# Performance work log

Hardware: AMD Instinct MI355X
Metric: run time of the kernel (lower is better)

The kernel has to match this reference:

```python
import jax, jax.numpy as jnp
import numpy as np

D = 256

def setup_inputs() -> dict:
    key = jax.random.key(0)
    ks = jax.random.split(key, 7)
    B, N = 4, 4096
    s = 1.0 / np.sqrt(D)
    return {
        "x": jax.random.normal(ks[0], (B, D, N), dtype=jnp.float32),
        "Wq": jax.random.normal(ks[1], (D, D), dtype=jnp.float32) * s,
        "bq": jax.random.normal(ks[2], (D,), dtype=jnp.float32) * s,
        "Wk": jax.random.normal(ks[3], (D, D), dtype=jnp.float32) * s,
        "bk": jax.random.normal(ks[4], (D,), dtype=jnp.float32) * s,
        "Wv": jax.random.normal(ks[5], (D, D), dtype=jnp.float32) * s,
        "bv": jax.random.normal(ks[6], (D,), dtype=jnp.float32) * s,
    }


def reference(x, Wq, bq, Wk, bk, Wv, bv):
    # x: (B, D, N) -> xt: (B, N, D)
    xt = jnp.swapaxes(x, 1, 2)
    q = xt @ Wq + bq  # (B, N, D)
    k = xt @ Wk + bk
    v = xt @ Wv + bv
    # full N x N attention, NO 1/sqrt(d) scaling (matches original)
    attn = jnp.einsum("bnd,bmd->bnm", q, k)
    attn = jax.nn.softmax(attn, axis=-1)
    out = jnp.einsum("bnm,bmd->bnd", attn, v)  # (B, N, D)
    return jnp.swapaxes(out, 1, 2)  # (B, D, N)
```

## Files before the change

### kernel.cpp

```cpp
#include <hip/hip_runtime.h>
#include <math.h>

#define Dd 256
#define Nn 4096
#define Bb 4
#define BQ 128
#define BK 128
#define SPLIT 2

typedef _Float16 f16;
typedef _Float16 half8 __attribute__((ext_vector_type(8)));
typedef _Float16 half4 __attribute__((ext_vector_type(4)));
typedef float f32x4 __attribute__((ext_vector_type(4)));

#define LOG2E 1.4426950408889634f

template <int CTRL>
__device__ __forceinline__ float dppf(float x) {
    int r = __builtin_amdgcn_update_dpp(0, __builtin_bit_cast(int, x),
                                        CTRL, 0xF, 0xF, false);
    return __builtin_bit_cast(float, r);
}
__device__ __forceinline__ float red16_max(float x) {
    x = fmaxf(x, dppf<0x128>(x));
    x = fmaxf(x, dppf<0x124>(x));
    x = fmaxf(x, dppf<0x122>(x));
    x = fmaxf(x, dppf<0x121>(x));
    return x;
}
__device__ __forceinline__ float red16_sum(float x) {
    x += dppf<0x128>(x); x += dppf<0x124>(x);
    x += dppf<0x122>(x); x += dppf<0x121>(x);
    return x;
}

__global__ __launch_bounds__(256) void wtrans(
    const float* __restrict__ Wq, const float* __restrict__ Wk,
    const float* __restrict__ Wv, f16* __restrict__ Wt)
{
    __shared__ float ld[64][65];
    const int which = blockIdx.y;
    const float* W = which == 0 ? Wq : (which == 1 ? Wk : Wv);
    const int tr = (blockIdx.x >> 2) * 64;
    const int tc = (blockIdx.x & 3) * 64;
    const int t = threadIdx.x;
    #pragma unroll
    for (int i = 0; i < 16; ++i) {
        int u = t + i * 256, r = u >> 6, c = u & 63;
        ld[r][c] = W[(size_t)(tr + r) * Dd + tc + c];
    }
    __syncthreads();
    f16* Wo = Wt + (size_t)which * Dd * Dd;
    #pragma unroll
    for (int i = 0; i < 16; ++i) {
        int u = t + i * 256, cp = u >> 6, rp = u & 63;
        Wo[(size_t)(tc + cp) * Dd + tr + rp] = (f16)ld[rp][cp];
    }
}

__global__ __launch_bounds__(256, 2) void qkv_mfma(
    const float* __restrict__ x, const f16* __restrict__ Wt,
    const float* __restrict__ bq, const float* __restrict__ bk,
    const float* __restrict__ bv,
    f16* __restrict__ Qh, f16* __restrict__ Kh, f16* __restrict__ Vth)
{
    __shared__ f16 xT[64][264];
    __shared__ float bs[256];
    const int t = threadIdx.x;
    const int wave = t >> 6, lane = t & 63, quad = lane >> 4, l15 = lane & 15;
    const int n0 = blockIdx.x * 64;
    const int b = blockIdx.y, which = blockIdx.z;
    const float* bias = which == 0 ? bq : (which == 1 ? bk : bv);
    bs[t] = bias[t];

    const float* xb = x + (size_t)b * Dd * Nn;
    #pragma unroll
    for (int i = 0; i < 16; ++i) {
        int u = t + i * 256, d = u >> 4, nq = (u & 15) * 4;
        float4 v4 = *(const float4*)&xb[(size_t)d * Nn + n0 + nq];
        xT[nq + 0][d] = (f16)v4.x; xT[nq + 1][d] = (f16)v4.y;
        xT[nq + 2][d] = (f16)v4.z; xT[nq + 3][d] = (f16)v4.w;
    }
    __syncthreads();

    half8 a[8];
    #pragma unroll
    for (int c = 0; c < 8; ++c)
        a[c] = *(const half8*)&xT[16 * wave + l15][c * 32 + quad * 8];

    f32x4 acc[16];
    #pragma unroll
    for (int dt = 0; dt < 16; ++dt) acc[dt] = (f32x4){0.f, 0.f, 0.f, 0.f};

    const f16* Wb = Wt + (size_t)which * Dd * Dd + (size_t)l15 * Dd + quad * 8;
    #pragma unroll
    for (int c = 0; c < 8; ++c) {
        #pragma unroll
        for (int dt = 0; dt < 16; ++dt) {
            half8 bfr = *(const half8*)(Wb + (size_t)dt * 16 * Dd + c * 32);
            acc[dt] = __builtin_amdgcn_mfma_f32_16x16x32_f16(a[c], bfr, acc[dt], 0, 0, 0);
        }
    }

    const int nrow = n0 + 16 * wave + quad * 4;
    if (which < 2) {
        f16* O = (which == 0 ? Qh : Kh) + ((size_t)b * Nn + nrow) * Dd;
        #pragma unroll
        for (int dt = 0; dt < 16; ++dt) {
            int col = dt * 16 + l15;
            float bvv = bs[col];
            #pragma unroll
            for (int r = 0; r < 4; ++r)
                O[(size_t)r * Dd + col] = (f16)(acc[dt][r] + bvv);
        }
    } else {
        f16* O = Vth + (size_t)b * Dd * Nn;
        #pragma unroll
        for (int dt = 0; dt < 16; ++dt) {
            int col = dt * 16 + l15;
            float bvv = bs[col];
            half4 o;
            #pragma unroll
            for (int r = 0; r < 4; ++r) o[r] = (f16)(acc[dt][r] + bvv);
            *(half4*)&O[(size_t)col * Nn + nrow] = o;
        }
    }
}

__global__ __launch_bounds__(512, 2) void attn_mfma(
    const f16* __restrict__ Qh, const f16* __restrict__ Kh,
    const f16* __restrict__ Vth, f16* __restrict__ Opart,
    float* __restrict__ mpart, float* __restrict__ lpart)
{
    __shared__ f16 Ks[BK][264];
    __shared__ f16 Ps[8][16][136];
    __shared__ float alpha_s[8][16];
    __shared__ float l_sh[8][16];

    const int t    = threadIdx.x;
    const int wave = t >> 6, lane = t & 63;
    const int quad = lane >> 4, l15 = lane & 15;
    const int b    = blockIdx.y;
    const int s    = blockIdx.z;
    const int q0   = blockIdx.x * BQ;
    const int qw   = q0 + wave * 16;
    const int kv0  = s * (Nn / SPLIT);

    half8 qf[8];
    const f16* Qrow = Qh + ((size_t)b * Nn + qw + l15) * Dd + quad * 8;
    #pragma unroll
    for (int c = 0; c < 8; ++c) {
        qf[c] = *(const half8*)(Qrow + c * 32);
        qf[c] = qf[c] * (f16)LOG2E;
    }

    f32x4 acc[16];
    #pragma unroll
    for (int n = 0; n < 16; ++n) acc[n] = (f32x4){0.f, 0.f, 0.f, 0.f};
    f32x4 m4 = {-1e30f, -1e30f, -1e30f, -1e30f};
    f32x4 l4 = {0.f, 0.f, 0.f, 0.f};

    const f16* Kb   = Kh + (size_t)b * Nn * Dd;
    const f16* Vrow = Vth + (size_t)b * Dd * Nn
                    + (size_t)(wave * 32 + l15) * Nn + quad * 8;

    for (int k0 = kv0; k0 < kv0 + Nn / SPLIT; k0 += BK) {
        half8 vbf[2][4];
        #pragma unroll
        for (int dt = 0; dt < 2; ++dt) {
            #pragma unroll
            for (int cbb = 0; cbb < 4; ++cbb)
                vbf[dt][cbb] = *(const half8*)(Vrow + (size_t)dt * 16 * Nn + k0 + cbb * 32);
        }

        __syncthreads();

        #pragma unroll
        for (int i = 0; i < 8; ++i) {
            int u = t + i * 512;
            int r = u >> 5, c = u & 31;
            *(half8*)&Ks[r][c * 8] =
                *(const half8*)(Kb + (size_t)(k0 + r) * Dd + c * 8);
        }
        __syncthreads();

        f32x4 S[8];
        #pragma unroll
        for (int cb = 0; cb < 8; ++cb) S[cb] = (f32x4){0.f, 0.f, 0.f, 0.f};
        #pragma unroll
        for (int c = 0; c < 8; ++c) {
            #pragma unroll
            for (int cb = 0; cb < 8; ++cb) {
                half8 kb = *(const half8*)&Ks[cb * 16 + l15][c * 32 + quad * 8];
                S[cb] = __builtin_amdgcn_mfma_f32_16x16x32_f16(qf[c], kb, S[cb], 0, 0, 0);
            }
        }

        f32x4 tmax = S[0];
        #pragma unroll
        for (int cb = 1; cb < 8; ++cb) {
            tmax.x = fmaxf(tmax.x, S[cb].x); tmax.y = fmaxf(tmax.y, S[cb].y);
            tmax.z = fmaxf(tmax.z, S[cb].z); tmax.w = fmaxf(tmax.w, S[cb].w);
        }
        tmax.x = red16_max(tmax.x); tmax.y = red16_max(tmax.y);
        tmax.z = red16_max(tmax.z); tmax.w = red16_max(tmax.w);
        f32x4 newm;
        newm.x = fmaxf(m4.x, tmax.x); newm.y = fmaxf(m4.y, tmax.y);
        newm.z = fmaxf(m4.z, tmax.z); newm.w = fmaxf(m4.w, tmax.w);
        f32x4 al;
        al.x = __builtin_amdgcn_exp2f(m4.x - newm.x);
        al.y = __builtin_amdgcn_exp2f(m4.y - newm.y);
        al.z = __builtin_amdgcn_exp2f(m4.z - newm.z);
        al.w = __builtin_amdgcn_exp2f(m4.w - newm.w);
        f32x4 P[8];
        #pragma unroll
        for (int cb = 0; cb < 8; ++cb) {
            P[cb].x = __builtin_amdgcn_exp2f(S[cb].x - newm.x);
            P[cb].y = __builtin_amdgcn_exp2f(S[cb].y - newm.y);
            P[cb].z = __builtin_amdgcn_exp2f(S[cb].z - newm.z);
            P[cb].w = __builtin_amdgcn_exp2f(S[cb].w - newm.w);
        }
        f32x4 rsum = P[0];
        #pragma unroll
        for (int cb = 1; cb < 8; ++cb) rsum += P[cb];
        rsum.x = red16_sum(rsum.x); rsum.y = red16_sum(rsum.y);
        rsum.z = red16_sum(rsum.z); rsum.w = red16_sum(rsum.w);
        l4 = l4 * al + rsum;
        m4 = newm;

        const int pr = quad * 4;
        #pragma unroll
        for (int cb = 0; cb < 8; ++cb) {
            Ps[wave][pr + 0][cb * 16 + l15] = (f16)P[cb].x;
            Ps[wave][pr + 1][cb * 16 + l15] = (f16)P[cb].y;
            Ps[wave][pr + 2][cb * 16 + l15] = (f16)P[cb].z;
            Ps[wave][pr + 3][cb * 16 + l15] = (f16)P[cb].w;
        }
        if (l15 == 0) {
            float4 a4 = {al.x, al.y, al.z, al.w};
            *(float4*)&alpha_s[wave][pr] = a4;
        }
        __syncthreads();

        float4 alq[8];
        int need = 0;
        #pragma unroll
        for (int qb = 0; qb < 8; ++qb) {
            alq[qb] = *(const float4*)&alpha_s[qb][pr];
            need |= (alq[qb].x != 1.f) | (alq[qb].y != 1.f) |
                    (alq[qb].z != 1.f) | (alq[qb].w != 1.f);
        }
        if (__any(need)) {
            #pragma unroll
            for (int qb = 0; qb < 8; ++qb) {
                f32x4 a = {alq[qb].x, alq[qb].y, alq[qb].z, alq[qb].w};
                acc[qb * 2 + 0] *= a;
                acc[qb * 2 + 1] *= a;
            }
        }

        #pragma unroll
        for (int qb = 0; qb < 8; ++qb) {
            #pragma unroll
            for (int cbb = 0; cbb < 4; ++cbb) {
                half8 ap = *(const half8*)&Ps[qb][l15][cbb * 32 + quad * 8];
                acc[qb * 2 + 0] = __builtin_amdgcn_mfma_f32_16x16x32_f16(
                    ap, vbf[0][cbb], acc[qb * 2 + 0], 0, 0, 0);
                acc[qb * 2 + 1] = __builtin_amdgcn_mfma_f32_16x16x32_f16(
                    ap, vbf[1][cbb], acc[qb * 2 + 1], 0, 0, 0);
            }
        }
    }

    __syncthreads();
    if (l15 == 0) {
        const int pr = quad * 4;
        float4 lv = {l4.x, l4.y, l4.z, l4.w};
        *(float4*)&l_sh[wave][pr] = lv;
        float mv[4] = {m4.x, m4.y, m4.z, m4.w};
        float lvv[4] = {l4.x, l4.y, l4.z, l4.w};
        #pragma unroll
        for (int r = 0; r < 4; ++r) {
            int n = qw + pr + r;
            mpart[(size_t)(s * Bb + b) * Nn + n] = mv[r];
            lpart[(size_t)(s * Bb + b) * Nn + n] = lvv[r];
        }
    }
    __syncthreads();

    f16* Ob = Opart + (size_t)(s * Bb + b) * Dd * Nn;
    #pragma unroll
    for (int qb = 0; qb < 8; ++qb) {
        float4 lq = *(const float4*)&l_sh[qb][quad * 4];
        f32x4 inv = {1.f / lq.x, 1.f / lq.y, 1.f / lq.z, 1.f / lq.w};
        #pragma unroll
        for (int dt = 0; dt < 2; ++dt) {
            int d = wave * 32 + dt * 16 + l15;
            f32x4 o = acc[qb * 2 + dt] * inv;
            half4 oh;
            oh[0] = (f16)o.x; oh[1] = (f16)o.y; oh[2] = (f16)o.z; oh[3] = (f16)o.w;
            *(half4*)&Ob[(size_t)d * Nn + q0 + qb * 16 + quad * 4] = oh;
        }
    }
}

__global__ __launch_bounds__(256) void combine(
    const f16* __restrict__ Opart, const float* __restrict__ mpart,
    const float* __restrict__ lpart, float* __restrict__ out)
{
    const int t = threadIdx.x;
    const int n0 = (blockIdx.x * 256 + t) * 8;
    const int d = blockIdx.y, b = blockIdx.z;

    float m[SPLIT][8], l[SPLIT][8];
    #pragma unroll
    for (int s = 0; s < SPLIT; ++s) {
        size_t base = (size_t)(s * Bb + b) * Nn + n0;
        float4 a0 = *(const float4*)&mpart[base];
        float4 a1 = *(const float4*)&mpart[base + 4];
        float4 c0 = *(const float4*)&lpart[base];
        float4 c1 = *(const float4*)&lpart[base + 4];
        m[s][0]=a0.x; m[s][1]=a0.y; m[s][2]=a0.z; m[s][3]=a0.w;
        m[s][4]=a1.x; m[s][5]=a1.y; m[s][6]=a1.z; m[s][7]=a1.w;
        l[s][0]=c0.x; l[s][1]=c0.y; l[s][2]=c0.z; l[s][3]=c0.w;
        l[s][4]=c1.x; l[s][5]=c1.y; l[s][6]=c1.z; l[s][7]=c1.w;
    }
    float w[SPLIT][8];
    #pragma unroll
    for (int jx = 0; jx < 8; ++jx) {
        float M = m[0][jx];
        #pragma unroll
        for (int s = 1; s < SPLIT; ++s) M = fmaxf(M, m[s][jx]);
        float L = 0.f;
        #pragma unroll
        for (int s = 0; s < SPLIT; ++s) {
            float ws = l[s][jx] * __builtin_amdgcn_exp2f(m[s][jx] - M);
            w[s][jx] = ws; L += ws;
        }
        float invL = 1.f / L;
        #pragma unroll
        for (int s = 0; s < SPLIT; ++s) w[s][jx] *= invL;
    }

    float o[8];
    #pragma unroll
    for (int jx = 0; jx < 8; ++jx) o[jx] = 0.f;
    #pragma unroll
    for (int s = 0; s < SPLIT; ++s) {
        half8 h = *(const half8*)&Opart[((size_t)(s * Bb + b) * Dd + d) * Nn + n0];
        #pragma unroll
        for (int jx = 0; jx < 8; ++jx) o[jx] += w[s][jx] * (float)h[jx];
    }
    float* op = out + ((size_t)b * Dd + d) * Nn + n0;
    f32x4 o0 = {o[0], o[1], o[2], o[3]};
    f32x4 o1 = {o[4], o[5], o[6], o[7]};
    *(f32x4*)op = o0;
    *(f32x4*)(op + 4) = o1;
}

extern "C" void kernel_launch(void* const* d_in, const int* in_sizes, int n_in,
                              void* d_out, int out_size, void* d_ws, size_t ws_size,
                              hipStream_t stream) {
    const float* x  = (const float*)d_in[0];
    const float* Wq = (const float*)d_in[1];
    const float* bq = (const float*)d_in[2];
    const float* Wk = (const float*)d_in[3];
    const float* bk = (const float*)d_in[4];
    const float* Wv = (const float*)d_in[5];
    const float* bv = (const float*)d_in[6];
    float* out = (float*)d_out;

    f16* Qh    = (f16*)d_ws;
    f16* Kh    = Qh + (size_t)Bb * Nn * Dd;
    f16* Vth   = Kh + (size_t)Bb * Nn * Dd;
    f16* Wt    = Vth + (size_t)Bb * Nn * Dd;
    f16* Opart = Wt + (size_t)3 * Dd * Dd;
    float* mpart = (float*)(Opart + (size_t)SPLIT * Bb * Dd * Nn);
    float* lpart = mpart + (size_t)SPLIT * Bb * Nn;

    wtrans<<<dim3(16, 3), 256, 0, stream>>>(Wq, Wk, Wv, Wt);
    qkv_mfma<<<dim3(Nn / 64, Bb, 3), 256, 0, stream>>>(
        x, Wt, bq, bk, bv, Qh, Kh, Vth);
    attn_mfma<<<dim3(Nn / BQ, Bb, SPLIT), 512, 0, stream>>>(
        Qh, Kh, Vth, Opart, mpart, lpart);
    combine<<<dim3(Nn / 2048, Dd, Bb), 256, 0, stream>>>(
        Opart, mpart, lpart, out);
}
```

Baseline: 251.9 us.

## Fuse Q/K/V projections into one kernel reusing x tile and staging W in LDS

Replaces the three-way split QKV projection kernel with a single 512-thread kernel per (n-tile, batch) that loads and converts the x tile once, then loops over Wq/Wk/Wv. Each weight matrix is staged into shared memory (aliased with the x transpose buffer) so B-fragments come from LDS instead of uncoalesced global reads, and waves split the output columns in halves. This removes the triple reading of x and the redundant global weight fetches. The cost is fewer blocks in the grid, one block per CU from the launch bounds, extra barriers, and a large LDS footprint.

```diff
diff --git a/kernel.cpp b/kernel.cpp
--- a/kernel.cpp
+++ b/kernel.cpp
@@ -58,25 +58,29 @@
     }
 }
 
-__global__ __launch_bounds__(256, 2) void qkv_mfma(
+__global__ __launch_bounds__(512, 1) void qkv_fused(
     const float* __restrict__ x, const f16* __restrict__ Wt,
     const float* __restrict__ bq, const float* __restrict__ bk,
     const float* __restrict__ bv,
     f16* __restrict__ Qh, f16* __restrict__ Kh, f16* __restrict__ Vth)
 {
-    __shared__ f16 xT[64][264];
-    __shared__ float bs[256];
+    __shared__ __align__(16) f16 Ws[256][264];
+    __shared__ float bs3[3][256];
+    f16 (*xT)[264] = (f16 (*)[264])&Ws[0][0];
+
     const int t = threadIdx.x;
     const int wave = t >> 6, lane = t & 63, quad = lane >> 4, l15 = lane & 15;
+    const int g = wave & 3;
+    const int h = wave >> 2;
     const int n0 = blockIdx.x * 64;
-    const int b = blockIdx.y, which = blockIdx.z;
-    const float* bias = which == 0 ? bq : (which == 1 ? bk : bv);
-    bs[t] = bias[t];
+    const int b = blockIdx.y;
+
+    if (t < 256) { bs3[0][t] = bq[t]; bs3[1][t] = bk[t]; bs3[2][t] = bv[t]; }
 
     const float* xb = x + (size_t)b * Dd * Nn;
     #pragma unroll
-    for (int i = 0; i < 16; ++i) {
-        int u = t + i * 256, d = u >> 4, nq = (u & 15) * 4;
+    for (int i = 0; i < 8; ++i) {
+        int u = t + i * 512, d = u >> 4, nq = (u & 15) * 4;
         float4 v4 = *(const float4*)&xb[(size_t)d * Nn + n0 + nq];
         xT[nq + 0][d] = (f16)v4.x; xT[nq + 1][d] = (f16)v4.y;
         xT[nq + 2][d] = (f16)v4.z; xT[nq + 3][d] = (f16)v4.w;
@@ -86,43 +90,55 @@
     half8 a[8];
     #pragma unroll
     for (int c = 0; c < 8; ++c)
-        a[c] = *(const half8*)&xT[16 * wave + l15][c * 32 + quad * 8];
-
-    f32x4 acc[16];
-    #pragma unroll
-    for (int dt = 0; dt < 16; ++dt) acc[dt] = (f32x4){0.f, 0.f, 0.f, 0.f};
-
-    const f16* Wb = Wt + (size_t)which * Dd * Dd + (size_t)l15 * Dd + quad * 8;
-    #pragma unroll
-    for (int c = 0; c < 8; ++c) {
-        #pragma unroll
-        for (int dt = 0; dt < 16; ++dt) {
-            half8 bfr = *(const half8*)(Wb + (size_t)dt * 16 * Dd + c * 32);
-            acc[dt] = __builtin_amdgcn_mfma_f32_16x16x32_f16(a[c], bfr, acc[dt], 0, 0, 0);
-        }
-    }
-
-    const int nrow = n0 + 16 * wave + quad * 4;
-    if (which < 2) {
-        f16* O = (which == 0 ? Qh : Kh) + ((size_t)b * Nn + nrow) * Dd;
-        #pragma unroll
-        for (int dt = 0; dt < 16; ++dt) {
-            int col = dt * 16 + l15;
-            float bvv = bs[col];
-            #pragma unroll
-            for (int r = 0; r < 4; ++r)
-                O[(size_t)r * Dd + col] = (f16)(acc[dt][r] + bvv);
-        }
-    } else {
-        f16* O = Vth + (size_t)b * Dd * Nn;
-        #pragma unroll
-        for (int dt = 0; dt < 16; ++dt) {
-            int col = dt * 16 + l15;
-            float bvv = bs[col];
-            half4 o;
-            #pragma unroll
-            for (int r = 0; r < 4; ++r) o[r] = (f16)(acc[dt][r] + bvv);
-            *(half4*)&O[(size_t)col * Nn + nrow] = o;
+        a[c] = *(const half8*)&xT[16 * g + l15][c * 32 + quad * 8];
+
+    const int nrow = n0 + 16 * g + quad * 4;
+
+    for (int which = 0; which < 3; ++which) {
+        __syncthreads();
+
+        const f16* Wb = Wt + (size_t)which * Dd * Dd;
+        #pragma unroll
+        for (int i = 0; i < 16; ++i) {
+            int u = t + i * 512;
+            int r = u >> 5, c = u & 31;
+            *(half8*)&Ws[r][c * 8] = *(const half8*)(Wb + (size_t)r * Dd + c * 8);
+        }
+        __syncthreads();
+
+        f32x4 acc[8];
+        #pragma unroll
+        for (int dt = 0; dt < 8; ++dt) acc[dt] = (f32x4){0.f, 0.f, 0.f, 0.f};
+        #pragma unroll
+        for (int c = 0; c < 8; ++c) {
+            #pragma unroll
+            for (int dt = 0; dt < 8; ++dt) {
+                half8 bfr = *(const half8*)&Ws[h * 128 + dt * 16 + l15][c * 32 + quad * 8];
+                acc[dt] = __builtin_amdgcn_mfma_f32_16x16x32_f16(a[c], bfr, acc[dt], 0, 0, 0);
+            }
+        }
+
+        if (which < 2) {
+            f16* O = (which == 0 ? Qh : Kh) + ((size_t)b * Nn + nrow) * Dd;
+            #pragma unroll
+            for (int dt = 0; dt < 8; ++dt) {
+                int col = h * 128 + dt * 16 + l15;
+                float bvv = bs3[which][col];
+                #pragma unroll
+                for (int r = 0; r < 4; ++r)
+                    O[(size_t)r * Dd + col] = (f16)(acc[dt][r] + bvv);
+            }
+        } else {
+            f16* O = Vth + (size_t)b * Dd * Nn;
+            #pragma unroll
+            for (int dt = 0; dt < 8; ++dt) {
+                int col = h * 128 + dt * 16 + l15;
+                float bvv = bs3[2][col];
+                half4 o;
+                #pragma unroll
+                for (int r = 0; r < 4; ++r) o[r] = (f16)(acc[dt][r] + bvv);
+                *(half4*)&O[(size_t)col * Nn + nrow] = o;
+            }
         }
     }
 }
@@ -379,7 +395,7 @@
     float* lpart = mpart + (size_t)SPLIT * Bb * Nn;
 
     wtrans<<<dim3(16, 3), 256, 0, stream>>>(Wq, Wk, Wv, Wt);
-    qkv_mfma<<<dim3(Nn / 64, Bb, 3), 256, 0, stream>>>(
+    qkv_fused<<<dim3(Nn / 64, Bb), 512, 0, stream>>>(
         x, Wt, bq, bk, bv, Qh, Kh, Vth);
     attn_mfma<<<dim3(Nn / BQ, Bb, SPLIT), 512, 0, stream>>>(
         Qh, Kh, Vth, Opart, mpart, lpart);
```

Result: faster. 220.6 us (-12.4%).
